# Kernel optimization log

Hardware: AMD Instinct MI355X
Metric: run time of the kernel (lower is better)

The kernel has to match this reference:

```python
import jax, jax.numpy as jnp
import numpy as np

N_ROW, N_COL, RANK = 8192, 8192, 256

def setup_inputs() -> dict:
    key = jax.random.key(0)
    k1, k2, k3 = jax.random.split(key, 3)
    X = jax.random.normal(k1, (N_ROW, RANK), dtype=jnp.float32)
    Y = jax.random.normal(k2, (RANK, N_COL), dtype=jnp.float32)
    beta = jax.random.normal(k3, (1,), dtype=jnp.float32)
    return {"X": X, "Y": Y, "beta": beta}

def reference(X, Y, beta):
    # mathematically equal to torch.norm(X[:,None] - Y.T, dim=-1).
    x2 = jnp.sum(X * X, axis=1, keepdims=True)          # (n_row, 1)
    y2 = jnp.sum(Y * Y, axis=0, keepdims=True)          # (1, n_col)
    cross = X @ Y                                        # (n_row, n_col) GEMM
    d2 = jnp.maximum(x2 + y2 - 2.0 * cross, 0.0)
    norms = jnp.sqrt(d2)
    z = -norms + beta                                    # beta broadcasts (1,)
    return z
```

## Files before the change

### kernel.cpp

```cpp
#include <hip/hip_runtime.h>

#define NROW 8192
#define NCOL 8192
#define RANK 256

#define BM 128
#define BN 128
#define BK 64

typedef __bf16  bf16x8 __attribute__((ext_vector_type(8)));
typedef float   f32x4  __attribute__((ext_vector_type(4)));

__device__ __forceinline__ unsigned short f2bf(float f) {
    unsigned int u = __builtin_bit_cast(unsigned int, f);
    u += 0x7fffu + ((u >> 16) & 1u);
    return (unsigned short)(u >> 16);
}

__global__ __launch_bounds__(256) void prep_x(const float* __restrict__ X,
                                              unsigned short* __restrict__ Xb,
                                              float* __restrict__ x2) {
    const int row  = blockIdx.x * 4 + (threadIdx.x >> 6);
    const int lane = threadIdx.x & 63;
    const float4 v = ((const float4*)(X + (size_t)row * RANK))[lane];
    float s = v.x * v.x + v.y * v.y + v.z * v.z + v.w * v.w;
    ushort4 b;
    b.x = f2bf(v.x); b.y = f2bf(v.y); b.z = f2bf(v.z); b.w = f2bf(v.w);
    ((ushort4*)(Xb + (size_t)row * RANK))[lane] = b;
    #pragma unroll
    for (int off = 32; off > 0; off >>= 1) s += __shfl_down(s, off);
    if (lane == 0) x2[row] = s;
}

__global__ __launch_bounds__(256) void prep_y(const float* __restrict__ Y,
                                              unsigned short* __restrict__ Ybt,
                                              float* __restrict__ y2) {
    __shared__ float tile[64][65];
    __shared__ float part[256];
    const int t  = threadIdx.x;
    const int j0 = blockIdx.x * 64;
    const int tq = t >> 6;
    const int tl = t & 63;
    float acc = 0.f;
    for (int c = 0; c < 4; ++c) {
        const int k0 = c * 64;
        #pragma unroll
        for (int i = 0; i < 16; ++i) {
            const int kk = tq * 16 + i;
            const float v = Y[(size_t)(k0 + kk) * NCOL + j0 + tl];
            tile[kk][tl] = v;
            acc += v * v;
        }
        __syncthreads();
        #pragma unroll
        for (int i = 0; i < 16; ++i) {
            const int jj = tq * 16 + i;
            Ybt[(size_t)(j0 + jj) * RANK + k0 + tl] = f2bf(tile[tl][jj]);
        }
        __syncthreads();
    }
    part[t] = acc;
    __syncthreads();
    if (t < 64)
        y2[j0 + t] = part[t] + part[t + 64] + part[t + 128] + part[t + 192];
}

__global__ __launch_bounds__(256, 2)
void l2_gemm(const unsigned short* __restrict__ A,
             const unsigned short* __restrict__ Bt,
             const float* __restrict__ x2,
             const float* __restrict__ y2,
             const float* __restrict__ beta_p,
             float* __restrict__ out) {
    __shared__ alignas(16) unsigned short As[BM * BK];
    __shared__ alignas(16) unsigned short Bs[BN * BK];

    const int t    = threadIdx.x;
    const int wid  = t >> 6;
    const int lane = t & 63;
    const int rowBase = blockIdx.x * BM;
    const int colBase = blockIdx.y * BN;

    const int waveM = (wid >> 1) * 64;
    const int waveN = (wid & 1) * 64;

    f32x4 acc[4][4] = {};

    const int lrow = lane >> 3;
    const int lcol = (lane & 7) * 8;

    for (int kt = 0; kt < RANK; kt += BK) {
        #pragma unroll
        for (int r = 0; r < 4; ++r) {
            const int rrel = r * 32 + wid * 8;
            const unsigned short* gp =
                A + (size_t)(rowBase + rrel + lrow) * RANK + kt + lcol;
            unsigned short* lp = As + rrel * BK;
            __builtin_amdgcn_global_load_lds(
                (__attribute__((address_space(1))) void*)gp,
                (__attribute__((address_space(3))) void*)lp, 16, 0, 0);
        }
        #pragma unroll
        for (int r = 0; r < 4; ++r) {
            const int rrel = r * 32 + wid * 8;
            const unsigned short* gp =
                Bt + (size_t)(colBase + rrel + lrow) * RANK + kt + lcol;
            unsigned short* lp = Bs + rrel * BK;
            __builtin_amdgcn_global_load_lds(
                (__attribute__((address_space(1))) void*)gp,
                (__attribute__((address_space(3))) void*)lp, 16, 0, 0);
        }
        __syncthreads();

        #pragma unroll
        for (int ks = 0; ks < BK; ks += 32) {
            const int kfrag = ks + (lane >> 4) * 8;
            bf16x8 af[4], bfr[4];
            #pragma unroll
            for (int mt = 0; mt < 4; ++mt)
                af[mt] = *(const bf16x8*)(As + (waveM + mt * 16 + (lane & 15)) * BK + kfrag);
            #pragma unroll
            for (int nt = 0; nt < 4; ++nt)
                bfr[nt] = *(const bf16x8*)(Bs + (waveN + nt * 16 + (lane & 15)) * BK + kfrag);
            #pragma unroll
            for (int mt = 0; mt < 4; ++mt)
                #pragma unroll
                for (int nt = 0; nt < 4; ++nt)
                    acc[mt][nt] = __builtin_amdgcn_mfma_f32_16x16x32_bf16(
                        af[mt], bfr[nt], acc[mt][nt], 0, 0, 0);
        }
        __syncthreads();
    }

    const float beta = *beta_p;
    const int cRow0 = rowBase + waveM + (lane >> 4) * 4;
    const int cCol0 = colBase + waveN + (lane & 15);
    #pragma unroll
    for (int nt = 0; nt < 4; ++nt) {
        const int   col = cCol0 + nt * 16;
        const float yv  = y2[col];
        #pragma unroll
        for (int mt = 0; mt < 4; ++mt) {
            #pragma unroll
            for (int r = 0; r < 4; ++r) {
                const int row = cRow0 + mt * 16 + r;
                float d2 = x2[row] + yv - 2.0f * acc[mt][nt][r];
                d2 = d2 > 0.f ? d2 : 0.f;
                out[(size_t)row * NCOL + col] = beta - sqrtf(d2);
            }
        }
    }
}

extern "C" void kernel_launch(void* const* d_in, const int* in_sizes, int n_in,
                              void* d_out, int out_size, void* d_ws, size_t ws_size,
                              hipStream_t stream) {
    const float* X    = (const float*)d_in[0];
    const float* Y    = (const float*)d_in[1];
    const float* beta = (const float*)d_in[2];
    float* out = (float*)d_out;

    char* ws = (char*)d_ws;
    unsigned short* Xb  = (unsigned short*)(ws);
    unsigned short* Ybt = (unsigned short*)(ws + (size_t)4 * 1024 * 1024);
    float* x2 = (float*)(ws + (size_t)8 * 1024 * 1024);
    float* y2 = (float*)(ws + (size_t)8 * 1024 * 1024 + 32 * 1024);

    prep_x<<<NROW / 4, 256, 0, stream>>>(X, Xb, x2);
    prep_y<<<NCOL / 64, 256, 0, stream>>>(Y, Ybt, y2);

    dim3 grid(NROW / BM, NCOL / BN);
    l2_gemm<<<grid, 256, 0, stream>>>(Xb, Ybt, x2, y2, beta, out);
}
```

Before: 349.0 us.

## Drop LDS staging, load MFMA fragments from global, remap blocks per XCD, nontemporal stores

```diff
diff --git a/kernel.cpp b/kernel.cpp
--- a/kernel.cpp
+++ b/kernel.cpp
@@ -6,7 +6,6 @@
 
 #define BM 128
 #define BN 128
-#define BK 64
 
 typedef __bf16  bf16x8 __attribute__((ext_vector_type(8)));
 typedef float   f32x4  __attribute__((ext_vector_type(4)));
@@ -65,89 +64,70 @@
         y2[j0 + t] = part[t] + part[t + 64] + part[t + 128] + part[t + 192];
 }
 
-__global__ __launch_bounds__(256, 2)
+__global__ __launch_bounds__(256, 3)
 void l2_gemm(const unsigned short* __restrict__ A,
              const unsigned short* __restrict__ Bt,
              const float* __restrict__ x2,
              const float* __restrict__ y2,
              const float* __restrict__ beta_p,
              float* __restrict__ out) {
-    __shared__ alignas(16) unsigned short As[BM * BK];
-    __shared__ alignas(16) unsigned short Bs[BN * BK];
-
     const int t    = threadIdx.x;
     const int wid  = t >> 6;
     const int lane = t & 63;
-    const int rowBase = blockIdx.x * BM;
-    const int colBase = blockIdx.y * BN;
 
-    const int waveM = (wid >> 1) * 64;
-    const int waveN = (wid & 1) * 64;
+    const int bid = blockIdx.x;
+    const int xcd = bid & 7;
+    const int loc = bid >> 3;
+    const int tx  = xcd * 8 + (loc & 7);
+    const int ty  = loc >> 3;
+
+    const int rowBase = tx * BM + (wid >> 1) * 64;
+    const int colBase = ty * BN + (wid & 1) * 64;
+
+    const int frow = lane & 15;
+    const int fk   = (lane >> 4) * 8;
+
+    const unsigned short* Ap = A  + (size_t)(rowBase + frow) * RANK + fk;
+    const unsigned short* Bp = Bt + (size_t)(colBase + frow) * RANK + fk;
 
     f32x4 acc[4][4] = {};
 
-    const int lrow = lane >> 3;
-    const int lcol = (lane & 7) * 8;
-
-    for (int kt = 0; kt < RANK; kt += BK) {
+    #pragma unroll
+    for (int ks = 0; ks < RANK; ks += 32) {
+        bf16x8 af[4], bfr[4];
         #pragma unroll
-        for (int r = 0; r < 4; ++r) {
-            const int rrel = r * 32 + wid * 8;
-            const unsigned short* gp =
-                A + (size_t)(rowBase + rrel + lrow) * RANK + kt + lcol;
-            unsigned short* lp = As + rrel * BK;
-            __builtin_amdgcn_global_load_lds(
-                (__attribute__((address_space(1))) void*)gp,
-                (__attribute__((address_space(3))) void*)lp, 16, 0, 0);
-        }
+        for (int mt = 0; mt < 4; ++mt)
+            af[mt] = *(const bf16x8*)(Ap + (size_t)(mt * 16) * RANK + ks);
         #pragma unroll
-        for (int r = 0; r < 4; ++r) {
-            const int rrel = r * 32 + wid * 8;
-            const unsigned short* gp =
-                Bt + (size_t)(colBase + rrel + lrow) * RANK + kt + lcol;
-            unsigned short* lp = Bs + rrel * BK;
-            __builtin_amdgcn_global_load_lds(
-                (__attribute__((address_space(1))) void*)gp,
-                (__attribute__((address_space(3))) void*)lp, 16, 0, 0);
-        }
-        __syncthreads();
-
+        for (int nt = 0; nt < 4; ++nt)
+            bfr[nt] = *(const bf16x8*)(Bp + (size_t)(nt * 16) * RANK + ks);
         #pragma unroll
-        for (int ks = 0; ks < BK; ks += 32) {
-            const int kfrag = ks + (lane >> 4) * 8;
-            bf16x8 af[4], bfr[4];
-            #pragma unroll
-            for (int mt = 0; mt < 4; ++mt)
-                af[mt] = *(const bf16x8*)(As + (waveM + mt * 16 + (lane & 15)) * BK + kfrag);
+        for (int mt = 0; mt < 4; ++mt)
             #pragma unroll
             for (int nt = 0; nt < 4; ++nt)
-                bfr[nt] = *(const bf16x8*)(Bs + (waveN + nt * 16 + (lane & 15)) * BK + kfrag);
-            #pragma unroll
-            for (int mt = 0; mt < 4; ++mt)
-                #pragma unroll
-                for (int nt = 0; nt < 4; ++nt)
-                    acc[mt][nt] = __builtin_amdgcn_mfma_f32_16x16x32_bf16(
-                        af[mt], bfr[nt], acc[mt][nt], 0, 0, 0);
-        }
-        __syncthreads();
+                acc[mt][nt] = __builtin_amdgcn_mfma_f32_16x16x32_bf16(
+                    af[mt], bfr[nt], acc[mt][nt], 0, 0, 0);
     }
 
     const float beta = *beta_p;
-    const int cRow0 = rowBase + waveM + (lane >> 4) * 4;
-    const int cCol0 = colBase + waveN + (lane & 15);
+    const int cRow0 = rowBase + (lane >> 4) * 4;
+    const int cCol0 = colBase + (lane & 15);
     #pragma unroll
     for (int nt = 0; nt < 4; ++nt) {
         const int   col = cCol0 + nt * 16;
         const float yv  = y2[col];
         #pragma unroll
         for (int mt = 0; mt < 4; ++mt) {
+            const float xv = x2[cRow0 + mt * 16];
             #pragma unroll
             for (int r = 0; r < 4; ++r) {
                 const int row = cRow0 + mt * 16 + r;
                 float d2 = x2[row] + yv - 2.0f * acc[mt][nt][r];
                 d2 = d2 > 0.f ? d2 : 0.f;
-                out[(size_t)row * NCOL + col] = beta - sqrtf(d2);
+                __builtin_nontemporal_store(beta - sqrtf(d2),
+                                            &out[(size_t)row * NCOL + col]);
             }
+            (void)xv;
         }
     }
 }
@@ -169,6 +149,5 @@
     prep_x<<<NROW / 4, 256, 0, stream>>>(X, Xb, x2);
     prep_y<<<NCOL / 64, 256, 0, stream>>>(Y, Ybt, y2);
 
-    dim3 grid(NROW / BM, NCOL / BN);
-    l2_gemm<<<grid, 256, 0, stream>>>(Xb, Ybt, x2, y2, beta, out);
+    l2_gemm<<<(NROW / BM) * (NCOL / BN), 256, 0, stream>>>(Xb, Ybt, x2, y2, beta, out);
 }
```

Measured after the change: 396.3 us. 13.5% more time.
